# Performance work log

Hardware: AMD Instinct MI355X
Metric: run time of the kernel (lower is better)

## Reference

```python
import jax, jax.numpy as jnp
import numpy as np

TOPK = 20
EPS = 1e-5  # torch BatchNorm1d default eps


def _segment_softmax(logits, seg, num_segments):
    m = jax.ops.segment_max(logits, seg, num_segments=num_segments)
    e = jnp.exp(logits - m[seg])
    s = jax.ops.segment_sum(e, seg, num_segments=num_segments)
    return e / (s[seg] + 1e-16)


def _forward(data, emb, W_lin, att_i, att_j, att_em_i, att_em_j, bias_gnn,
             W_ff, b_ff, bn1_g, bn1_b, bn2_g, bn2_b, W_out, b_out):
    B, N, F = data.shape
    H, D = att_i.shape
    BN = B * N
    x = data.reshape(BN, F)

    # --- dynamic top-k cosine-similarity graph (original detaches embeddings) ---
    w = jax.lax.stop_gradient(emb)
    nrm = jnp.linalg.norm(w, axis=-1, keepdims=True)  # (N,1)
    cos = (w @ w.T) / (nrm * nrm.T)                   # (N,N)
    _, topk_idx = jax.lax.top_k(cos, TOPK)            # (N,K)

    src = topk_idx.reshape(-1)                        # j (source of message)
    tgt = jnp.repeat(jnp.arange(N), TOPK)             # i (target)
    off = (jnp.arange(B) * N)[:, None]                # batch the edge list
    src_b = (src[None, :] + off).reshape(-1)          # (B*N*K,)
    tgt_b = (tgt[None, :] + off).reshape(-1)
    # remove_self_loops then add_self_loops: mask topk self-edges, append loops
    self_mask = src_b == tgt_b
    loops = jnp.arange(BN)
    src_all = jnp.concatenate([src_b, loops])         # (E,)
    tgt_all = jnp.concatenate([tgt_b, loops])
    dead = jnp.concatenate([self_mask, jnp.zeros(BN, dtype=bool)])

    # --- GraphLayer: GAT-style attention with node embeddings in the keys ---
    xh = (x @ W_lin).reshape(BN, H, D)                # lin(x), per head
    emb_full = jnp.tile(emb, (B, 1))                  # (BN, D) repeated per batch
    # per-node attention scores; key_i = [x_i || emb_i] . [att_i || att_em_i]
    score_i = jnp.einsum('nhd,hd->nh', xh, att_i) + emb_full @ att_em_i.T  # (BN,H)
    score_j = jnp.einsum('nhd,hd->nh', xh, att_j) + emb_full @ att_em_j.T
    alpha = score_i[tgt_all] + score_j[src_all]       # (E,H)
    alpha = jax.nn.leaky_relu(alpha, 0.2)
    alpha = jnp.where(dead[:, None], -1e30, alpha)    # drop removed self-edges
    alpha = _segment_softmax(alpha, tgt_all, BN)      # softmax over in-edges of i
    msgs = xh[src_all] * alpha[:, :, None]            # (E,H,D)
    agg = jax.ops.segment_sum(msgs, tgt_all, num_segments=BN)  # (BN,H,D)
    out = agg.reshape(BN, H * D) + bias_gnn           # concat heads + bias

    # --- GNNLayer head: linear -> BatchNorm1d (train stats) -> relu ---
    out = out @ W_ff + b_ff                           # (BN, D)
    mu = out.mean(0)
    var = out.var(0)
    out = (out - mu) / jnp.sqrt(var + EPS) * bn1_g + bn1_b
    out = jax.nn.relu(out)

    # --- multiply by embeddings, channelwise BN, relu (dropout: eval = identity) ---
    h = out.reshape(B, N, D) * emb[None]              # (B,N,D)
    mu2 = h.mean(axis=(0, 1))
    var2 = h.var(axis=(0, 1))
    h = (h - mu2) / jnp.sqrt(var2 + EPS) * bn2_g + bn2_b
    h = jax.nn.relu(h)

    # --- OutLayer (layer_num=1): single linear per node ---
    return h @ W_out + b_out                          # (B, N, out_win)


def setup_inputs() -> dict:
    key = jax.random.key(0)
    ks = jax.random.split(key, 12)
    B, N, F, D, H, OW = 16, 2000, 128, 64, 4, 200
    s = 0.05
    return {
        'data': jax.random.normal(ks[0], (B, N, F), jnp.float32),
        'emb': jax.random.normal(ks[1], (N, D), jnp.float32),
        'W_lin': jax.random.normal(ks[2], (F, H * D), jnp.float32) * s,
        'att_i': jax.random.normal(ks[3], (H, D), jnp.float32) * s,
        'att_j': jax.random.normal(ks[4], (H, D), jnp.float32) * s,
        'att_em_i': jax.random.normal(ks[5], (H, D), jnp.float32) * s,
        'att_em_j': jax.random.normal(ks[6], (H, D), jnp.float32) * s,
        'bias_gnn': jnp.zeros((H * D,), jnp.float32),
        'W_ff': jax.random.normal(ks[7], (H * D, D), jnp.float32) * s,
        'b_ff': jnp.zeros((D,), jnp.float32),
        'bn1_g': jnp.ones((D,), jnp.float32),
        'bn1_b': jnp.zeros((D,), jnp.float32),
        'bn2_g': jnp.ones((D,), jnp.float32),
        'bn2_b': jnp.zeros((D,), jnp.float32),
        'W_out': jax.random.normal(ks[8], (D, OW), jnp.float32) * s,
        'b_out': jnp.zeros((OW,), jnp.float32),
    }


def reference(data, emb, W_lin, att_i, att_j, att_em_i, att_em_j, bias_gnn,
              W_ff, b_ff, bn1_g, bn1_b, bn2_g, bn2_b, W_out, b_out):
    return _forward(data, emb, W_lin, att_i, att_j, att_em_i, att_em_j, bias_gnn,
                    W_ff, b_ff, bn1_g, bn1_b, bn2_g, bn2_b, W_out, b_out)
```

## Files before the change

kernel.cpp:

```cpp
#include <hip/hip_runtime.h>
#include <math.h>

#define B_   16
#define N_   2000
#define F_   128
#define D_   64
#define H_   4
#define OW_  200
#define K_   20
#define BN_  (B_*N_)
#define HD_  (H_*D_)
#define EPS_ 1e-5f
#define NP_  2048

__global__ __launch_bounds__(256) void k_norms(const float* __restrict__ emb,
                                               float* __restrict__ nrm) {
    int i = blockIdx.x * blockDim.x + threadIdx.x;
    if (i < N_) {
        const float* e = emb + (size_t)i * D_;
        float s = 0.f;
        #pragma unroll
        for (int d = 0; d < D_; ++d) s += e[d] * e[d];
        nrm[i] = sqrtf(s);
    } else if (i < NP_) {
        nrm[i] = 1.f;
    }
}

__global__ __launch_bounds__(256) void k_trans(const float* __restrict__ emb,
                                               float* __restrict__ embT) {
    int idx = blockIdx.x * 256 + threadIdx.x;
    int k = idx >> 11, j = idx & (NP_ - 1);
    float v = (j < N_) ? emb[(size_t)j * D_ + k] : 0.f;
    embT[idx] = v;
}

__global__ __launch_bounds__(256) void k_cos(const float* __restrict__ emb,
                                             const float* __restrict__ embT,
                                             const float* __restrict__ nrm,
                                             float* __restrict__ cosm) {
    const int t    = threadIdx.x;
    const int i0   = blockIdx.y * 16;
    const int r0   = (t >> 6) * 4;
    const int lane = t & 63;
    const int j4   = blockIdx.x * 256 + lane * 4;

    __shared__ float eL[16 * D_];
    for (int idx = t; idx < 16 * D_; idx += 256)
        eL[idx] = emb[(size_t)i0 * D_ + idx];
    __syncthreads();

    float acc[4][4];
    #pragma unroll
    for (int r = 0; r < 4; ++r)
        #pragma unroll
        for (int cc = 0; cc < 4; ++cc) acc[r][cc] = 0.f;

    for (int k4 = 0; k4 < D_; k4 += 4) {
        float es[4][4];
        #pragma unroll
        for (int r = 0; r < 4; ++r) {
            float4 ev = *(const float4*)&eL[(r0 + r) * D_ + k4];
            es[r][0] = ev.x; es[r][1] = ev.y; es[r][2] = ev.z; es[r][3] = ev.w;
        }
        #pragma unroll
        for (int kk = 0; kk < 4; ++kk) {
            float4 b = *(const float4*)&embT[(size_t)(k4 + kk) * NP_ + j4];
            #pragma unroll
            for (int r = 0; r < 4; ++r) {
                acc[r][0] = fmaf(es[r][kk], b.x, acc[r][0]);
                acc[r][1] = fmaf(es[r][kk], b.y, acc[r][1]);
                acc[r][2] = fmaf(es[r][kk], b.z, acc[r][2]);
                acc[r][3] = fmaf(es[r][kk], b.w, acc[r][3]);
            }
        }
    }

    float4 nj = *(const float4*)&nrm[j4];
    #pragma unroll
    for (int r = 0; r < 4; ++r) {
        float ni = nrm[i0 + r0 + r];
        float4 o;
        o.x = acc[r][0] / (ni * nj.x);
        o.y = acc[r][1] / (ni * nj.y);
        o.z = acc[r][2] / (ni * nj.z);
        o.w = acc[r][3] / (ni * nj.w);
        *(float4*)&cosm[(size_t)(i0 + r0 + r) * NP_ + j4] = o;
    }
}

__device__ __forceinline__ unsigned long long kmax64(unsigned long long a,
                                                     unsigned long long b) {
    return a > b ? a : b;
}

__global__ __launch_bounds__(256) void k_sel(const float* __restrict__ cosm,
                                             int* __restrict__ topk) {
    const int t    = threadIdx.x;
    const int lane = t & 63;
    const int i    = blockIdx.x * 4 + (t >> 6);
    const float* row = cosm + (size_t)i * NP_;

    unsigned long long key[32];
    #pragma unroll
    for (int m = 0; m < 8; ++m) {
        float4 b = *(const float4*)&row[m * 256 + lane * 4];
        float vv[4] = {b.x, b.y, b.z, b.w};
        #pragma unroll
        for (int q = 0; q < 4; ++q) {
            const int s = m * 4 + q;
            const int j = m * 256 + lane * 4 + q;
            unsigned int x  = __float_as_uint(vv[q]);
            unsigned int mv = (x & 0x80000000u) ? ~x : (x | 0x80000000u);
            unsigned long long kk =
                ((unsigned long long)mv << 32) | (unsigned int)(NP_ - 1 - j);
            key[s] = (j < N_) ? kk : 0ull;
        }
    }

    unsigned long long loc;
    {
        unsigned long long l1[16];
        #pragma unroll
        for (int s = 0; s < 16; ++s) l1[s] = kmax64(key[s], key[s + 16]);
        unsigned long long l2[8];
        #pragma unroll
        for (int s = 0; s < 8; ++s) l2[s] = kmax64(l1[s], l1[s + 8]);
        unsigned long long l3[4];
        #pragma unroll
        for (int s = 0; s < 4; ++s) l3[s] = kmax64(l2[s], l2[s + 4]);
        loc = kmax64(kmax64(l3[0], l3[2]), kmax64(l3[1], l3[3]));
    }

    for (int k = 0; k < K_; ++k) {
        unsigned long long w = loc;
        #pragma unroll
        for (int off = 1; off < 64; off <<= 1)
            w = kmax64(w, __shfl_xor(w, off, 64));

        if (lane == 0)
            topk[i * K_ + k] = (NP_ - 1) - (int)(unsigned int)(w & 0xFFFFFFFFu);

        #pragma unroll
        for (int s = 0; s < 32; ++s)
            if (key[s] == w) key[s] = 0ull;
        {
            unsigned long long l1[16];
            #pragma unroll
            for (int s = 0; s < 16; ++s) l1[s] = kmax64(key[s], key[s + 16]);
            unsigned long long l2[8];
            #pragma unroll
            for (int s = 0; s < 8; ++s) l2[s] = kmax64(l1[s], l1[s + 8]);
            unsigned long long l3[4];
            #pragma unroll
            for (int s = 0; s < 4; ++s) l3[s] = kmax64(l2[s], l2[s + 4]);
            loc = kmax64(kmax64(l3[0], l3[2]), kmax64(l3[1], l3[3]));
        }
    }
}

__global__ __launch_bounds__(256) void k_lin(const float* __restrict__ x,
                                             const float* __restrict__ Wlin,
                                             const float* __restrict__ emb,
                                             const float* __restrict__ atti,
                                             const float* __restrict__ attj,
                                             const float* __restrict__ attei,
                                             const float* __restrict__ attej,
                                             float* __restrict__ xh,
                                             float* __restrict__ si,
                                             float* __restrict__ sj) {
    const int t  = threadIdx.x;
    const int n0 = blockIdx.x * 16;
    const int i0 = n0 % N_;
    const int r0 = (t >> 6) * 4;
    const int c4 = (t & 63) * 4;

    __shared__ float xL[16 * F_];

    for (int idx = t; idx < 16 * F_; idx += 256)
        xL[idx] = x[(size_t)n0 * F_ + idx];
    __syncthreads();

    float acc[4][4];
    #pragma unroll
    for (int r = 0; r < 4; ++r)
        #pragma unroll
        for (int cc = 0; cc < 4; ++cc) acc[r][cc] = 0.f;

    for (int k4 = 0; k4 < F_; k4 += 4) {
        float xs[4][4];
        #pragma unroll
        for (int r = 0; r < 4; ++r) {
            float4 xv = *(const float4*)&xL[(r0 + r) * F_ + k4];
            xs[r][0] = xv.x; xs[r][1] = xv.y; xs[r][2] = xv.z; xs[r][3] = xv.w;
        }
        #pragma unroll
        for (int kk = 0; kk < 4; ++kk) {
            float4 w = *(const float4*)&Wlin[(size_t)(k4 + kk) * HD_ + c4];
            #pragma unroll
            for (int r = 0; r < 4; ++r) {
                acc[r][0] = fmaf(xs[r][kk], w.x, acc[r][0]);
                acc[r][1] = fmaf(xs[r][kk], w.y, acc[r][1]);
                acc[r][2] = fmaf(xs[r][kk], w.z, acc[r][2]);
                acc[r][3] = fmaf(xs[r][kk], w.w, acc[r][3]);
            }
        }
    }

    #pragma unroll
    for (int r = 0; r < 4; ++r) {
        float4 o; o.x = acc[r][0]; o.y = acc[r][1]; o.z = acc[r][2]; o.w = acc[r][3];
        *(float4*)&xh[(size_t)(n0 + r0 + r) * HD_ + c4] = o;
    }

    const int h  = (t & 63) >> 4;
    const int de = 4 * (t & 15);
    float4 ai4  = *(const float4*)&atti[c4];
    float4 aj4  = *(const float4*)&attj[c4];
    float4 aei4 = *(const float4*)&attei[c4];
    float4 aej4 = *(const float4*)&attej[c4];
    #pragma unroll
    for (int r = 0; r < 4; ++r) {
        float4 e4 = *(const float4*)&emb[(size_t)(i0 + r0 + r) * D_ + de];
        float vi = acc[r][0] * ai4.x + e4.x * aei4.x
                 + acc[r][1] * ai4.y + e4.y * aei4.y
                 + acc[r][2] * ai4.z + e4.z * aei4.z
                 + acc[r][3] * ai4.w + e4.w * aei4.w;
        float vj = acc[r][0] * aj4.x + e4.x * aej4.x
                 + acc[r][1] * aj4.y + e4.y * aej4.y
                 + acc[r][2] * aj4.z + e4.z * aej4.z
                 + acc[r][3] * aj4.w + e4.w * aej4.w;
        #pragma unroll
        for (int off = 1; off < 16; off <<= 1) {
            vi += __shfl_xor(vi, off);
            vj += __shfl_xor(vj, off);
        }
        if ((t & 15) == 0) {
            si[(size_t)(n0 + r0 + r) * H_ + h] = vi;
            sj[(size_t)(n0 + r0 + r) * H_ + h] = vj;
        }
    }
}

#define RA_ 8
__global__ __launch_bounds__(256) void k_attn(const float* __restrict__ xh,
                                              const float* __restrict__ si,
                                              const float* __restrict__ sj,
                                              const int* __restrict__ topk,
                                              const float* __restrict__ biasg,
                                              const float* __restrict__ Wff,
                                              const float* __restrict__ bff,
                                              float* __restrict__ out2) {
    const int t   = threadIdx.x;
    const int nwg = BN_ / RA_;
    const int swz = (blockIdx.x & 7) * (nwg >> 3) + (blockIdx.x >> 3);
    const int n0  = swz * RA_;
    __shared__ int   srcL[RA_][21];
    __shared__ float wA[RA_][H_][21];
    __shared__ float aggL[RA_][HD_];
    __shared__ float pL[4][RA_][D_];

    if (t < RA_ * 21) {
        const int r = t / 21, e = t % 21;
        const int n = n0 + r;
        const int i = n % N_;
        const int b = n / N_;
        int s; bool dead = false;
        if (e < K_) { int kk = topk[i * K_ + e]; s = b * N_ + kk; dead = (kk == i); }
        else        { s = n; }
        srcL[r][e] = s;
        #pragma unroll
        for (int h = 0; h < H_; ++h) {
            float a = si[(size_t)n * H_ + h] + sj[(size_t)s * H_ + h];
            a = a > 0.f ? a : 0.2f * a;
            if (dead) a = -1e30f;
            wA[r][h][e] = a;
        }
    }
    __syncthreads();

    if (t < RA_ * H_) {
        const int r = t >> 2, h = t & 3;
        float m = -3e38f;
        for (int e = 0; e < 21; ++e) m = fmaxf(m, wA[r][h][e]);
        float sum = 0.f;
        for (int e = 0; e < 21; ++e) { float ex = expf(wA[r][h][e] - m); wA[r][h][e] = ex; sum += ex; }
        float inv = 1.f / (sum + 1e-16f);
        for (int e = 0; e < 21; ++e) wA[r][h][e] *= inv;
    }
    __syncthreads();

    {
        const int g = t >> 6, lane = t & 63, c4 = lane * 4, h = lane >> 4;
        #pragma unroll
        for (int rr = 0; rr < 2; ++rr) {
            const int r = g * 2 + rr;
            float a0 = 0.f, a1 = 0.f, a2 = 0.f, a3 = 0.f;
            for (int e = 0; e < 21; ++e) {
                float wv = wA[r][h][e];
                float4 xv = *(const float4*)&xh[(size_t)srcL[r][e] * HD_ + c4];
                a0 = fmaf(wv, xv.x, a0); a1 = fmaf(wv, xv.y, a1);
                a2 = fmaf(wv, xv.z, a2); a3 = fmaf(wv, xv.w, a3);
            }
            float4 bg = *(const float4*)&biasg[c4];
            float4 o; o.x = a0 + bg.x; o.y = a1 + bg.y; o.z = a2 + bg.z; o.w = a3 + bg.w;
            *(float4*)&aggL[r][c4] = o;
        }
    }
    __syncthreads();

    {
        const int g = t >> 6, d = t & 63;
        float accf[RA_];
        #pragma unroll
        for (int r = 0; r < RA_; ++r) accf[r] = 0.f;
        for (int c4 = g * 64; c4 < g * 64 + 64; c4 += 4) {
            float as[RA_][4];
            #pragma unroll
            for (int r = 0; r < RA_; ++r) {
                float4 av = *(const float4*)&aggL[r][c4];
                as[r][0] = av.x; as[r][1] = av.y; as[r][2] = av.z; as[r][3] = av.w;
            }
            #pragma unroll
            for (int kk = 0; kk < 4; ++kk) {
                float w = Wff[(size_t)(c4 + kk) * D_ + d];
                #pragma unroll
                for (int r = 0; r < RA_; ++r) accf[r] = fmaf(as[r][kk], w, accf[r]);
            }
        }
        #pragma unroll
        for (int r = 0; r < RA_; ++r) pL[g][r][d] = accf[r];
    }
    __syncthreads();

    {
        const int r0 = (t >> 6) * 2, d = t & 63;
        #pragma unroll
        for (int rr = 0; rr < 2; ++rr) {
            const int r = r0 + rr;
            float o = pL[0][r][d] + pL[1][r][d] + pL[2][r][d] + pL[3][r][d] + bff[d];
            out2[(size_t)(n0 + r) * D_ + d] = o;
        }
    }
}

__global__ __launch_bounds__(256) void k_red1(const float* __restrict__ out2,
                                              double* __restrict__ S,
                                              double* __restrict__ SS) {
    const int t = threadIdx.x;
    double s = 0.0, ss = 0.0;
    const int total = BN_ * D_;
    for (int idx = blockIdx.x * 256 + t; idx < total; idx += gridDim.x * 256) {
        float v = out2[idx];
        s += v; ss += (double)v * v;
    }
    __shared__ double sb[256], ssb[256];
    sb[t] = s; ssb[t] = ss;
    __syncthreads();
    if (t < 64) {
        double a = sb[t] + sb[t + 64] + sb[t + 128] + sb[t + 192];
        double b = ssb[t] + ssb[t + 64] + ssb[t + 128] + ssb[t + 192];
        atomicAdd(&S[t], a);
        atomicAdd(&SS[t], b);
    }
}

__global__ __launch_bounds__(256) void k_bn1(const float* __restrict__ out2,
                                             const float* __restrict__ emb,
                                             const double* __restrict__ S1,
                                             const double* __restrict__ SS1,
                                             const float* __restrict__ g1,
                                             const float* __restrict__ b1,
                                             float* __restrict__ hb,
                                             double* __restrict__ S2,
                                             double* __restrict__ SS2) {
    const int t = threadIdx.x;
    __shared__ float scale[64], shift[64];
    if (t < 64) {
        double mu  = S1[t] / (double)BN_;
        double var = SS1[t] / (double)BN_ - mu * mu;
        float rstd = rsqrtf((float)var + EPS_);
        float sc   = rstd * g1[t];
        scale[t] = sc;
        shift[t] = b1[t] - (float)mu * sc;
    }
    __syncthreads();
    const int d = t & 63;
    double s = 0.0, ss = 0.0;
    const int total = BN_ * D_;
    for (int idx = blockIdx.x * 256 + t; idx < total; idx += gridDim.x * 256) {
        float v = out2[idx];
        v = v * scale[d] + shift[d];
        v = fmaxf(v, 0.f);
        int n = idx >> 6;
        int i = n % N_;
        v *= emb[(size_t)i * D_ + d];
        hb[idx] = v;
        s += v; ss += (double)v * v;
    }
    __shared__ double sb[256], ssb[256];
    sb[t] = s; ssb[t] = ss;
    __syncthreads();
    if (t < 64) {
        double a = sb[t] + sb[t + 64] + sb[t + 128] + sb[t + 192];
        double b = ssb[t] + ssb[t + 64] + ssb[t + 128] + ssb[t + 192];
        atomicAdd(&S2[t], a);
        atomicAdd(&SS2[t], b);
    }
}

__global__ __launch_bounds__(256) void k_out(const float* __restrict__ hb,
                                             const double* __restrict__ S2,
                                             const double* __restrict__ SS2,
                                             const float* __restrict__ g2,
                                             const float* __restrict__ b2,
                                             const float* __restrict__ Wout,
                                             const float* __restrict__ bout,
                                             float* __restrict__ out) {
    const int t  = threadIdx.x;
    const int n0 = blockIdx.x * 16;
    __shared__ float scale[64], shift[64];
    __shared__ float hL[16 * D_];
    if (t < 64) {
        double mu  = S2[t] / (double)BN_;
        double var = SS2[t] / (double)BN_ - mu * mu;
        float rstd = rsqrtf((float)var + EPS_);
        float sc   = rstd * g2[t];
        scale[t] = sc;
        shift[t] = b2[t] - (float)mu * sc;
    }
    __syncthreads();
    for (int idx = t; idx < 16 * D_; idx += 256) {
        float v = hb[(size_t)n0 * D_ + idx];
        int d = idx & 63;
        v = fmaxf(v * scale[d] + shift[d], 0.f);
        hL[idx] = v;
    }
    __syncthreads();
    if (t < OW_) {
        float acc[16];
        #pragma unroll
        for (int r = 0; r < 16; ++r) acc[r] = 0.f;
        for (int d4 = 0; d4 < D_; d4 += 4) {
            float hs[16][4];
            #pragma unroll
            for (int r = 0; r < 16; ++r) {
                float4 hv = *(const float4*)&hL[r * D_ + d4];
                hs[r][0] = hv.x; hs[r][1] = hv.y; hs[r][2] = hv.z; hs[r][3] = hv.w;
            }
            #pragma unroll
            for (int kk = 0; kk < 4; ++kk) {
                float w = Wout[(size_t)(d4 + kk) * OW_ + t];
                #pragma unroll
                for (int r = 0; r < 16; ++r) acc[r] = fmaf(hs[r][kk], w, acc[r]);
            }
        }
        float bo = bout[t];
        #pragma unroll
        for (int r = 0; r < 16; ++r) out[(size_t)(n0 + r) * OW_ + t] = acc[r] + bo;
    }
}

extern "C" void kernel_launch(void* const* d_in, const int* in_sizes, int n_in,
                              void* d_out, int out_size, void* d_ws, size_t ws_size,
                              hipStream_t stream) {
    const float* data  = (const float*)d_in[0];
    const float* emb   = (const float*)d_in[1];
    const float* Wlin  = (const float*)d_in[2];
    const float* atti  = (const float*)d_in[3];
    const float* attj  = (const float*)d_in[4];
    const float* attei = (const float*)d_in[5];
    const float* attej = (const float*)d_in[6];
    const float* biasg = (const float*)d_in[7];
    const float* Wff   = (const float*)d_in[8];
    const float* bff   = (const float*)d_in[9];
    const float* g1    = (const float*)d_in[10];
    const float* b1    = (const float*)d_in[11];
    const float* g2    = (const float*)d_in[12];
    const float* b2    = (const float*)d_in[13];
    const float* Wout  = (const float*)d_in[14];
    const float* bout  = (const float*)d_in[15];
    float* out = (float*)d_out;

    char* w = (char*)d_ws;
    size_t off = 0;
    auto alloc = [&](size_t bytes) -> void* {
        void* p = w + off;
        off += (bytes + 255) & ~(size_t)255;
        return p;
    };
    float*  nrm  = (float*) alloc((size_t)NP_ * sizeof(float));
    int*    topk = (int*)   alloc((size_t)N_ * K_ * sizeof(int));
    float*  xh   = (float*) alloc((size_t)BN_ * HD_ * sizeof(float));
    float*  embT = xh;
    float*  cosm = xh + (size_t)D_ * NP_;
    float*  si   = (float*) alloc((size_t)BN_ * H_ * sizeof(float));
    float*  sj   = (float*) alloc((size_t)BN_ * H_ * sizeof(float));
    float*  out2 = (float*) alloc((size_t)BN_ * D_ * sizeof(float));
    float*  hb   = (float*) alloc((size_t)BN_ * D_ * sizeof(float));
    double* S1   = (double*)alloc(64 * sizeof(double));
    double* SS1  = (double*)alloc(64 * sizeof(double));
    double* S2   = (double*)alloc(64 * sizeof(double));
    double* SS2  = (double*)alloc(64 * sizeof(double));

    hipMemsetAsync(S1, 0, 4 * 512, stream);

    hipLaunchKernelGGL(k_norms, dim3(8),            dim3(256), 0, stream, emb, nrm);
    hipLaunchKernelGGL(k_trans, dim3(D_*NP_/256),   dim3(256), 0, stream, emb, embT);
    hipLaunchKernelGGL(k_cos,   dim3(NP_/256, N_/16), dim3(256), 0, stream,
                       emb, embT, nrm, cosm);
    hipLaunchKernelGGL(k_sel,   dim3(N_/4),         dim3(256), 0, stream, cosm, topk);
    hipLaunchKernelGGL(k_lin,   dim3(BN_ / 16),     dim3(256), 0, stream,
                       data, Wlin, emb, atti, attj, attei, attej, xh, si, sj);
    hipLaunchKernelGGL(k_attn,  dim3(BN_ / RA_),    dim3(256), 0, stream,
                       xh, si, sj, topk, biasg, Wff, bff, out2);
    hipLaunchKernelGGL(k_red1,  dim3(128),          dim3(256), 0, stream, out2, S1, SS1);
    hipLaunchKernelGGL(k_bn1,   dim3(512),          dim3(256), 0, stream,
                       out2, emb, S1, SS1, g1, b1, hb, S2, SS2);
    hipLaunchKernelGGL(k_out,   dim3(BN_ / 16),     dim3(256), 0, stream,
                       hb, S2, SS2, g2, b2, Wout, bout, out);
}
```

Before: 283.0 us.

## Apply W_ff per head before aggregation and fold GNN bias into FF bias

Moves the feed-forward projection ahead of the attention aggregation. Each node's per-head features are multiplied by the matching W_ff slice in k_lin, giving yh, and k_attn then takes the alpha-weighted sum of yh and reduces across heads with shuffles. The GNN bias is folded into a precomputed bias2 (bias_gnn·W_ff + b_ff) inside a merged prep kernel that also absorbs the norms and transpose kernels. This removes the shared-memory FF matmul and two barriers from k_attn, at the cost of extra FLOPs in k_lin and a changed summation order; k_red1 also gets a larger grid.

```diff
diff --git a/kernel.cpp b/kernel.cpp
--- a/kernel.cpp
+++ b/kernel.cpp
@@ -13,26 +13,36 @@
 #define EPS_ 1e-5f
 #define NP_  2048
 
-__global__ __launch_bounds__(256) void k_norms(const float* __restrict__ emb,
-                                               float* __restrict__ nrm) {
-    int i = blockIdx.x * blockDim.x + threadIdx.x;
-    if (i < N_) {
-        const float* e = emb + (size_t)i * D_;
-        float s = 0.f;
-        #pragma unroll
-        for (int d = 0; d < D_; ++d) s += e[d] * e[d];
-        nrm[i] = sqrtf(s);
-    } else if (i < NP_) {
-        nrm[i] = 1.f;
-    }
-}
-
-__global__ __launch_bounds__(256) void k_trans(const float* __restrict__ emb,
-                                               float* __restrict__ embT) {
-    int idx = blockIdx.x * 256 + threadIdx.x;
-    int k = idx >> 11, j = idx & (NP_ - 1);
-    float v = (j < N_) ? emb[(size_t)j * D_ + k] : 0.f;
-    embT[idx] = v;
+__global__ __launch_bounds__(256) void k_prep(const float* __restrict__ emb,
+                                              const float* __restrict__ biasg,
+                                              const float* __restrict__ Wff,
+                                              const float* __restrict__ bff,
+                                              float* __restrict__ nrm,
+                                              float* __restrict__ embT,
+                                              float* __restrict__ bias2) {
+    const int t = threadIdx.x, b = blockIdx.x;
+    const int idx = b * 256 + t;
+    {
+        int k = idx >> 11, j = idx & (NP_ - 1);
+        embT[idx] = (j < N_) ? emb[(size_t)j * D_ + k] : 0.f;
+    }
+    if (b < 8) {
+        int i = idx;
+        if (i < N_) {
+            const float* e = emb + (size_t)i * D_;
+            float s = 0.f;
+            #pragma unroll
+            for (int d = 0; d < D_; ++d) s += e[d] * e[d];
+            nrm[i] = sqrtf(s);
+        } else if (i < NP_) {
+            nrm[i] = 1.f;
+        }
+    }
+    if (b == 8 && t < D_) {
+        float s = bff[t];
+        for (int c = 0; c < HD_; ++c) s = fmaf(biasg[c], Wff[(size_t)c * D_ + t], s);
+        bias2[t] = s;
+    }
 }
 
 __global__ __launch_bounds__(256) void k_cos(const float* __restrict__ emb,
@@ -166,16 +176,19 @@
                                              const float* __restrict__ attj,
                                              const float* __restrict__ attei,
                                              const float* __restrict__ attej,
-                                             float* __restrict__ xh,
+                                             const float* __restrict__ Wff,
+                                             float* __restrict__ yh,
                                              float* __restrict__ si,
                                              float* __restrict__ sj) {
     const int t  = threadIdx.x;
     const int n0 = blockIdx.x * 16;
     const int i0 = n0 % N_;
     const int r0 = (t >> 6) * 4;
-    const int c4 = (t & 63) * 4;
+    const int lane = t & 63;
+    const int c4 = lane * 4;
 
     __shared__ float xL[16 * F_];
+    __shared__ float xhL[16 * HD_];
 
     for (int idx = t; idx < 16 * F_; idx += 256)
         xL[idx] = x[(size_t)n0 * F_ + idx];
@@ -210,46 +223,91 @@
     #pragma unroll
     for (int r = 0; r < 4; ++r) {
         float4 o; o.x = acc[r][0]; o.y = acc[r][1]; o.z = acc[r][2]; o.w = acc[r][3];
-        *(float4*)&xh[(size_t)(n0 + r0 + r) * HD_ + c4] = o;
-    }
-
-    const int h  = (t & 63) >> 4;
-    const int de = 4 * (t & 15);
-    float4 ai4  = *(const float4*)&atti[c4];
-    float4 aj4  = *(const float4*)&attj[c4];
-    float4 aei4 = *(const float4*)&attei[c4];
-    float4 aej4 = *(const float4*)&attej[c4];
-    #pragma unroll
-    for (int r = 0; r < 4; ++r) {
-        float4 e4 = *(const float4*)&emb[(size_t)(i0 + r0 + r) * D_ + de];
-        float vi = acc[r][0] * ai4.x + e4.x * aei4.x
-                 + acc[r][1] * ai4.y + e4.y * aei4.y
-                 + acc[r][2] * ai4.z + e4.z * aei4.z
-                 + acc[r][3] * ai4.w + e4.w * aei4.w;
-        float vj = acc[r][0] * aj4.x + e4.x * aej4.x
-                 + acc[r][1] * aj4.y + e4.y * aej4.y
-                 + acc[r][2] * aj4.z + e4.z * aej4.z
-                 + acc[r][3] * aj4.w + e4.w * aej4.w;
-        #pragma unroll
-        for (int off = 1; off < 16; off <<= 1) {
-            vi += __shfl_xor(vi, off);
-            vj += __shfl_xor(vj, off);
-        }
-        if ((t & 15) == 0) {
-            si[(size_t)(n0 + r0 + r) * H_ + h] = vi;
-            sj[(size_t)(n0 + r0 + r) * H_ + h] = vj;
+        *(float4*)&xhL[(r0 + r) * HD_ + c4] = o;
+    }
+
+    {
+        const int h  = lane >> 4;
+        const int de = 4 * (t & 15);
+        float4 ai4  = *(const float4*)&atti[c4];
+        float4 aj4  = *(const float4*)&attj[c4];
+        float4 aei4 = *(const float4*)&attei[c4];
+        float4 aej4 = *(const float4*)&attej[c4];
+        #pragma unroll
+        for (int r = 0; r < 4; ++r) {
+            float4 e4 = *(const float4*)&emb[(size_t)(i0 + r0 + r) * D_ + de];
+            float vi = acc[r][0] * ai4.x + e4.x * aei4.x
+                     + acc[r][1] * ai4.y + e4.y * aei4.y
+                     + acc[r][2] * ai4.z + e4.z * aei4.z
+                     + acc[r][3] * ai4.w + e4.w * aei4.w;
+            float vj = acc[r][0] * aj4.x + e4.x * aej4.x
+                     + acc[r][1] * aj4.y + e4.y * aej4.y
+                     + acc[r][2] * aj4.z + e4.z * aej4.z
+                     + acc[r][3] * aj4.w + e4.w * aej4.w;
+            #pragma unroll
+            for (int off = 1; off < 16; off <<= 1) {
+                vi += __shfl_xor(vi, off);
+                vj += __shfl_xor(vj, off);
+            }
+            if ((t & 15) == 0) {
+                si[(size_t)(n0 + r0 + r) * H_ + h] = vi;
+                sj[(size_t)(n0 + r0 + r) * H_ + h] = vj;
+            }
+        }
+    }
+    __syncthreads();
+
+    {
+        const int h  = c4 >> 6;
+        const int d4 = c4 & 63;
+        float ya[4][4];
+        #pragma unroll
+        for (int r = 0; r < 4; ++r)
+            #pragma unroll
+            for (int cc = 0; cc < 4; ++cc) ya[r][cc] = 0.f;
+
+        for (int k4 = 0; k4 < D_; k4 += 4) {
+            float wf[4][4];
+            #pragma unroll
+            for (int kk = 0; kk < 4; ++kk) {
+                float4 w = *(const float4*)&Wff[(size_t)(h * D_ + k4 + kk) * D_ + d4];
+                wf[kk][0] = w.x; wf[kk][1] = w.y; wf[kk][2] = w.z; wf[kk][3] = w.w;
+            }
+            #pragma unroll
+            for (int r = 0; r < 4; ++r) {
+                float4 xv = *(const float4*)&xhL[(r0 + r) * HD_ + h * D_ + k4];
+                ya[r][0] = fmaf(xv.x, wf[0][0], ya[r][0]);
+                ya[r][1] = fmaf(xv.x, wf[0][1], ya[r][1]);
+                ya[r][2] = fmaf(xv.x, wf[0][2], ya[r][2]);
+                ya[r][3] = fmaf(xv.x, wf[0][3], ya[r][3]);
+                ya[r][0] = fmaf(xv.y, wf[1][0], ya[r][0]);
+                ya[r][1] = fmaf(xv.y, wf[1][1], ya[r][1]);
+                ya[r][2] = fmaf(xv.y, wf[1][2], ya[r][2]);
+                ya[r][3] = fmaf(xv.y, wf[1][3], ya[r][3]);
+                ya[r][0] = fmaf(xv.z, wf[2][0], ya[r][0]);
+                ya[r][1] = fmaf(xv.z, wf[2][1], ya[r][1]);
+                ya[r][2] = fmaf(xv.z, wf[2][2], ya[r][2]);
+                ya[r][3] = fmaf(xv.z, wf[2][3], ya[r][3]);
+                ya[r][0] = fmaf(xv.w, wf[3][0], ya[r][0]);
+                ya[r][1] = fmaf(xv.w, wf[3][1], ya[r][1]);
+                ya[r][2] = fmaf(xv.w, wf[3][2], ya[r][2]);
+                ya[r][3] = fmaf(xv.w, wf[3][3], ya[r][3]);
+            }
+        }
+        #pragma unroll
+        for (int r = 0; r < 4; ++r) {
+            float4 o; o.x = ya[r][0]; o.y = ya[r][1]; o.z = ya[r][2]; o.w = ya[r][3];
+            *(float4*)&yh[(size_t)(n0 + r0 + r) * HD_ + c4] = o;
         }
     }
 }
 
 #define RA_ 8
-__global__ __launch_bounds__(256) void k_attn(const float* __restrict__ xh,
+__global__ __launch_bounds__(256) void k_attn(const float* __restrict__ yh,
                                               const float* __restrict__ si,
                                               const float* __restrict__ sj,
                                               const int* __restrict__ topk,
-                                              const float* __restrict__ biasg,
-                                              const float* __restrict__ Wff,
-                                              const float* __restrict__ bff,
+                                              const float* __restrict__ bias2,
                                               float* __restrict__ out2) {
     const int t   = threadIdx.x;
     const int nwg = BN_ / RA_;
@@ -257,8 +315,6 @@
     const int n0  = swz * RA_;
     __shared__ int   srcL[RA_][21];
     __shared__ float wA[RA_][H_][21];
-    __shared__ float aggL[RA_][HD_];
-    __shared__ float pL[4][RA_][D_];
 
     if (t < RA_ * 21) {
         const int r = t / 21, e = t % 21;
@@ -298,48 +354,20 @@
             float a0 = 0.f, a1 = 0.f, a2 = 0.f, a3 = 0.f;
             for (int e = 0; e < 21; ++e) {
                 float wv = wA[r][h][e];
-                float4 xv = *(const float4*)&xh[(size_t)srcL[r][e] * HD_ + c4];
-                a0 = fmaf(wv, xv.x, a0); a1 = fmaf(wv, xv.y, a1);
-                a2 = fmaf(wv, xv.z, a2); a3 = fmaf(wv, xv.w, a3);
-            }
-            float4 bg = *(const float4*)&biasg[c4];
-            float4 o; o.x = a0 + bg.x; o.y = a1 + bg.y; o.z = a2 + bg.z; o.w = a3 + bg.w;
-            *(float4*)&aggL[r][c4] = o;
-        }
-    }
-    __syncthreads();
-
-    {
-        const int g = t >> 6, d = t & 63;
-        float accf[RA_];
-        #pragma unroll
-        for (int r = 0; r < RA_; ++r) accf[r] = 0.f;
-        for (int c4 = g * 64; c4 < g * 64 + 64; c4 += 4) {
-            float as[RA_][4];
-            #pragma unroll
-            for (int r = 0; r < RA_; ++r) {
-                float4 av = *(const float4*)&aggL[r][c4];
-                as[r][0] = av.x; as[r][1] = av.y; as[r][2] = av.z; as[r][3] = av.w;
-            }
-            #pragma unroll
-            for (int kk = 0; kk < 4; ++kk) {
-                float w = Wff[(size_t)(c4 + kk) * D_ + d];
-                #pragma unroll
-                for (int r = 0; r < RA_; ++r) accf[r] = fmaf(as[r][kk], w, accf[r]);
-            }
-        }
-        #pragma unroll
-        for (int r = 0; r < RA_; ++r) pL[g][r][d] = accf[r];
-    }
-    __syncthreads();
-
-    {
-        const int r0 = (t >> 6) * 2, d = t & 63;
-        #pragma unroll
-        for (int rr = 0; rr < 2; ++rr) {
-            const int r = r0 + rr;
-            float o = pL[0][r][d] + pL[1][r][d] + pL[2][r][d] + pL[3][r][d] + bff[d];
-            out2[(size_t)(n0 + r) * D_ + d] = o;
+                float4 yv = *(const float4*)&yh[(size_t)srcL[r][e] * HD_ + c4];
+                a0 = fmaf(wv, yv.x, a0); a1 = fmaf(wv, yv.y, a1);
+                a2 = fmaf(wv, yv.z, a2); a3 = fmaf(wv, yv.w, a3);
+            }
+            a0 += __shfl_xor(a0, 16); a0 += __shfl_xor(a0, 32);
+            a1 += __shfl_xor(a1, 16); a1 += __shfl_xor(a1, 32);
+            a2 += __shfl_xor(a2, 16); a2 += __shfl_xor(a2, 32);
+            a3 += __shfl_xor(a3, 16); a3 += __shfl_xor(a3, 32);
+            if (lane < 16) {
+                float4 b2 = *(const float4*)&bias2[lane * 4];
+                float4 o; o.x = a0 + b2.x; o.y = a1 + b2.y;
+                          o.z = a2 + b2.z; o.w = a3 + b2.w;
+                *(float4*)&out2[(size_t)(n0 + r) * D_ + lane * 4] = o;
+            }
         }
     }
 }
@@ -489,11 +517,12 @@
         off += (bytes + 255) & ~(size_t)255;
         return p;
     };
-    float*  nrm  = (float*) alloc((size_t)NP_ * sizeof(float));
-    int*    topk = (int*)   alloc((size_t)N_ * K_ * sizeof(int));
-    float*  xh   = (float*) alloc((size_t)BN_ * HD_ * sizeof(float));
-    float*  embT = xh;
-    float*  cosm = xh + (size_t)D_ * NP_;
+    float*  nrm   = (float*) alloc((size_t)NP_ * sizeof(float));
+    int*    topk  = (int*)   alloc((size_t)N_ * K_ * sizeof(int));
+    float*  bias2 = (float*) alloc((size_t)D_ * sizeof(float));
+    float*  yh   = (float*) alloc((size_t)BN_ * HD_ * sizeof(float));
+    float*  embT = yh;
+    float*  cosm = yh + (size_t)D_ * NP_;
     float*  si   = (float*) alloc((size_t)BN_ * H_ * sizeof(float));
     float*  sj   = (float*) alloc((size_t)BN_ * H_ * sizeof(float));
     float*  out2 = (float*) alloc((size_t)BN_ * D_ * sizeof(float));
@@ -505,18 +534,18 @@
 
     hipMemsetAsync(S1, 0, 4 * 512, stream);
 
-    hipLaunchKernelGGL(k_norms, dim3(8),            dim3(256), 0, stream, emb, nrm);
-    hipLaunchKernelGGL(k_trans, dim3(D_*NP_/256),   dim3(256), 0, stream, emb, embT);
+    hipLaunchKernelGGL(k_prep,  dim3(D_*NP_/256),    dim3(256), 0, stream,
+                       emb, biasg, Wff, bff, nrm, embT, bias2);
     hipLaunchKernelGGL(k_cos,   dim3(NP_/256, N_/16), dim3(256), 0, stream,
                        emb, embT, nrm, cosm);
-    hipLaunchKernelGGL(k_sel,   dim3(N_/4),         dim3(256), 0, stream, cosm, topk);
-    hipLaunchKernelGGL(k_lin,   dim3(BN_ / 16),     dim3(256), 0, stream,
-                       data, Wlin, emb, atti, attj, attei, attej, xh, si, sj);
-    hipLaunchKernelGGL(k_attn,  dim3(BN_ / RA_),    dim3(256), 0, stream,
-                       xh, si, sj, topk, biasg, Wff, bff, out2);
-    hipLaunchKernelGGL(k_red1,  dim3(128),          dim3(256), 0, stream, out2, S1, SS1);
-    hipLaunchKernelGGL(k_bn1,   dim3(512),          dim3(256), 0, stream,
+    hipLaunchKernelGGL(k_sel,   dim3(N_/4),          dim3(256), 0, stream, cosm, topk);
+    hipLaunchKernelGGL(k_lin,   dim3(BN_ / 16),      dim3(256), 0, stream,
+                       data, Wlin, emb, atti, attj, attei, attej, Wff, yh, si, sj);
+    hipLaunchKernelGGL(k_attn,  dim3(BN_ / RA_),     dim3(256), 0, stream,
+                       yh, si, sj, topk, bias2, out2);
+    hipLaunchKernelGGL(k_red1,  dim3(512),           dim3(256), 0, stream, out2, S1, SS1);
+    hipLaunchKernelGGL(k_bn1,   dim3(512),           dim3(256), 0, stream,
                        out2, emb, S1, SS1, g1, b1, hb, S2, SS2);
-    hipLaunchKernelGGL(k_out,   dim3(BN_ / 16),     dim3(256), 0, stream,
+    hipLaunchKernelGGL(k_out,   dim3(BN_ / 16),      dim3(256), 0, stream,
                        hb, S2, SS2, g2, b2, Wout, bout, out);
 }
```

New measurement: 287.3 us. Within noise of the previous version (+1.5%).
